# Optimization experiments

Measured on AMD Instinct MI355X. Metric: run time of the kernel, lower is better.

The kernel has to match this reference:

```python
import jax, jax.numpy as jnp
import numpy as np

EPS = 1e-5

def ln(x, g, b):
    m = x.mean(-1, keepdims=True)
    v = ((x - m) ** 2).mean(-1, keepdims=True)
    return (x - m) / jnp.sqrt(v + EPS) * g + b

def mha(x, in_w, in_b, out_w, out_b, nh):
    # Faithful nn.MultiheadAttention with batch_first=False: x is (L, B, D),
    # attention runs over axis 0 (sequence), axis 1 is batch.
    L, Bb, D = x.shape
    hd = D // nh
    qkv = x @ in_w.T + in_b                      # (L, B, 3D)
    q, k, v = jnp.split(qkv, 3, axis=-1)
    q = q.reshape(L, Bb, nh, hd) * (hd ** -0.5)
    k = k.reshape(L, Bb, nh, hd)
    v = v.reshape(L, Bb, nh, hd)
    a = jax.nn.softmax(jnp.einsum('lbhe,sbhe->bhls', q, k), axis=-1)
    o = jnp.einsum('bhls,sbhe->lbhe', a, v).reshape(L, Bb, D)
    return o @ out_w.T + out_b

def psb_forward(features, prev_slots,
                lnq_g, lnq_b, lnkv_g, lnkv_b,
                wq, wk, wv, wo,
                lnt_g, lnt_b, t_in_w, t_in_b, t_out_w, t_out_b,
                lno_g, lno_b, o_in_w, o_in_b, o_out_w, o_out_b,
                lnp_g, lnp_b, w1, b1, w2, b2):
    B, T, L, D = features.shape
    N = prev_slots.shape[2]
    nh = 1                                        # inverse_nh
    hd = D // nh
    slots = ln(prev_slots, lnq_g, lnq_b).reshape(B * T, N, D)
    xkv = ln(features, lnkv_g, lnkv_b).reshape(B * T, L, D)
    # ---- inverse cross attention (softmax over query/slot dim, renorm over keys) ----
    q = (slots @ wq.T).reshape(B * T, N, nh, hd).transpose(0, 2, 1, 3) * (D ** -0.5)
    k = (xkv @ wk.T).reshape(B * T, L, nh, hd).transpose(0, 2, 1, 3)
    v = (xkv @ wv.T).reshape(B * T, L, nh, hd).transpose(0, 2, 1, 3)
    attn = jnp.einsum('bhnd,bhsd->bhns', q, k)    # (BT, nh, N, L)
    attn = jax.nn.softmax(attn, axis=-2)          # over slots (queries)
    attn = attn / attn.sum(-1, keepdims=True)     # renormalize over keys
    s = jnp.einsum('bhns,bhsd->bnhd', attn, v).reshape(B * T, N, D) @ wo.T
    # ---- time attention: input (B*T, N, D); seq axis 0 = B*T, batch = N ----
    s = ln(s, lnt_g, lnt_b)
    s = mha(s, t_in_w, t_in_b, t_out_w, t_out_b, 4)
    # rearrange '(b t) n d -> (b n) t d'
    s = s.reshape(B, T, N, D).transpose(0, 2, 1, 3).reshape(B * N, T, D)
    # ---- object attention: seq axis 0 = B*N, batch = T ----
    s = ln(s, lno_g, lno_b)
    s = mha(s, o_in_w, o_in_b, o_out_w, o_out_b, 4)
    # faithful to torch .view(B, T, N, D) on a contiguous (B*N, T, D) tensor:
    # raw row-major reinterpretation (same as torch)
    s = s.reshape(B, T, N, D)
    # ---- FFN projection + residual with prev_slots ----
    s = ln(s, lnp_g, lnp_b)
    s = jax.nn.relu(s @ w1.T + b1) @ w2.T + b2
    return s + prev_slots

def setup_inputs() -> dict:
    key = jax.random.key(0)
    ks = jax.random.split(key, 16)
    B, T, L, D, N, F = 8, 16, 1024, 192, 8, 512
    w = lambda k, shape: jax.random.normal(k, shape, jnp.float32) * 0.02
    return {
        'features': jax.random.normal(ks[0], (B, T, L, D), jnp.float32),
        'prev_slots': jax.random.normal(ks[1], (B, T, N, D), jnp.float32),
        'lnq_g': jnp.ones((D,), jnp.float32), 'lnq_b': jnp.zeros((D,), jnp.float32),
        'lnkv_g': jnp.ones((D,), jnp.float32), 'lnkv_b': jnp.zeros((D,), jnp.float32),
        'wq': w(ks[2], (D, D)), 'wk': w(ks[3], (D, D)),
        'wv': w(ks[4], (D, D)), 'wo': w(ks[5], (D, D)),
        'lnt_g': jnp.ones((D,), jnp.float32), 'lnt_b': jnp.zeros((D,), jnp.float32),
        't_in_w': w(ks[6], (3 * D, D)), 't_in_b': jnp.zeros((3 * D,), jnp.float32),
        't_out_w': w(ks[7], (D, D)), 't_out_b': jnp.zeros((D,), jnp.float32),
        'lno_g': jnp.ones((D,), jnp.float32), 'lno_b': jnp.zeros((D,), jnp.float32),
        'o_in_w': w(ks[8], (3 * D, D)), 'o_in_b': jnp.zeros((3 * D,), jnp.float32),
        'o_out_w': w(ks[9], (D, D)), 'o_out_b': jnp.zeros((D,), jnp.float32),
        'lnp_g': jnp.ones((D,), jnp.float32), 'lnp_b': jnp.zeros((D,), jnp.float32),
        'w1': w(ks[10], (F, D)), 'b1': jnp.zeros((F,), jnp.float32),
        'w2': w(ks[11], (D, F)), 'b2': jnp.zeros((D,), jnp.float32),
    }

def reference(features, prev_slots,
              lnq_g, lnq_b, lnkv_g, lnkv_b,
              wq, wk, wv, wo,
              lnt_g, lnt_b, t_in_w, t_in_b, t_out_w, t_out_b,
              lno_g, lno_b, o_in_w, o_in_b, o_out_w, o_out_b,
              lnp_g, lnp_b, w1, b1, w2, b2):
    return psb_forward(features, prev_slots,
                       lnq_g, lnq_b, lnkv_g, lnkv_b,
                       wq, wk, wv, wo,
                       lnt_g, lnt_b, t_in_w, t_in_b, t_out_w, t_out_b,
                       lno_g, lno_b, o_in_w, o_in_b, o_out_w, o_out_b,
                       lnp_g, lnp_b, w1, b1, w2, b2)
```

## Files before the change

kernel.cpp:

```cpp
#include <hip/hip_runtime.h>
#include <hip/hip_bf16.h>
#include <stdint.h>

typedef __hip_bfloat16 bf16;

__device__ __forceinline__ float b2f(bf16 x){ return __bfloat162float(x); }
__device__ __forceinline__ bf16  f2b(float x){ return __float2bfloat16(x); }
__device__ __forceinline__ int dflag(const void* rawg){
  return *(const uint32_t*)rawg == 0x3F803F80u;
}

struct Ptrs26 { const void* p[26]; };
__global__ __launch_bounds__(256) void k_convert(Ptrs26 ps, float* __restrict__ dst){
  constexpr int kN[26] = {192,192,192,192, 36864,36864,36864,36864, 192,192,
                          110592,576, 36864,192, 192,192, 110592,576, 36864,192,
                          192,192, 98304,512, 98304,192};
  constexpr int kR[26] = {0,0,0,0, 0,0,0,0, 0,0,
                          576,0, 192,0, 0,0, 576,0, 192,0,
                          0,0, 512,0, 192,0};
  const int b = blockIdx.x;
  int tz = 0, boff = 0, off = 0;
  for (int i = 0; i < 26; ++i){
    const int nb = (kN[i] + 255) >> 8;
    if (b < boff + nb){ tz = i; break; }
    boff += nb; off += kN[i];
  }
  const int cnt = kN[tz];
  const int tid = (b - boff)*256 + threadIdx.x;
  if (tid >= cnt) return;
  const int flag = dflag(ps.p[0]);
  float v = flag ? b2f(((const bf16*)ps.p[tz])[tid]) : ((const float*)ps.p[tz])[tid];
  const int R = kR[tz];
  if (R == 0){
    dst[off + tid] = v;
  } else {
    const int K = cnt / R;
    int o = tid / K, e = tid - o*K;
    dst[off + e*R + o] = v;
  }
}

__global__ __launch_bounds__(192) void k_m1m2(
    const float* __restrict__ wq, const float* __restrict__ wk,
    const float* __restrict__ wo, const float* __restrict__ wv,
    float* __restrict__ M1, float* __restrict__ M2t)
{
  const int t = threadIdx.x, row = blockIdx.x, mat = blockIdx.y;
  float acc = 0.f;
  if (mat == 0){
    for (int d = 0; d < 192; ++d) acc += wq[d*192 + row] * wk[d*192 + t];
    M1[row*192 + t] = acc * 0.07216878364870323f;
  } else {
    for (int d = 0; d < 192; ++d) acc += wo[row*192 + d] * wv[d*192 + t];
    M2t[t*192 + row] = acc;
  }
}

__global__ __launch_bounds__(192) void k_qprime(
    const void* __restrict__ prev, const void* __restrict__ rawg,
    const float* __restrict__ g, const float* __restrict__ be,
    const float* __restrict__ M1, float* __restrict__ Qp)
{
  __shared__ float sRaw[8][196];
  __shared__ float sS[8][196];
  __shared__ float sMS[8][2];
  const int t = threadIdx.x, bt = blockIdx.x;
  const int flag = dflag(rawg);
  #pragma unroll
  for (int r = 0; r < 8; ++r){
    size_t idx = ((size_t)bt*8 + r)*192 + t;
    sRaw[r][t] = flag ? b2f(((const bf16*)prev)[idx]) : ((const float*)prev)[idx];
  }
  __syncthreads();
  if (t < 8){
    float s = 0.f, q = 0.f;
    for (int e = 0; e < 192; ++e){ float x = sRaw[t][e]; s += x; q += x*x; }
    float m = s*(1.f/192.f);
    float rstd = rsqrtf(q*(1.f/192.f) - m*m + 1e-5f);
    sMS[t][0] = m; sMS[t][1] = rstd;
  }
  __syncthreads();
  const float gg = g[t], bb = be[t];
  #pragma unroll
  for (int r = 0; r < 8; ++r)
    sS[r][t] = (sRaw[r][t] - sMS[r][0])*sMS[r][1]*gg + bb;
  __syncthreads();
  float acc[8] = {};
  for (int f = 0; f < 192; ++f){
    float mv = M1[f*192 + t];
    #pragma unroll
    for (int n = 0; n < 8; ++n) acc[n] += sS[n][f]*mv;
  }
  #pragma unroll
  for (int n = 0; n < 8; ++n) Qp[(size_t)bt*1536 + n*192 + t] = acc[n];
}

__global__ __launch_bounds__(256) void k_front(
    const void* __restrict__ feat, const void* __restrict__ rawg,
    const float* __restrict__ g, const float* __restrict__ be,
    const float* __restrict__ Qp, float* __restrict__ pP, float* __restrict__ pR)
{
  __shared__ float sX[16][196];
  __shared__ float sQ[8][196];
  __shared__ float sA[16][9];
  __shared__ float sRS[4][8];
  const int t = threadIdx.x, lane = t & 63, w = t >> 6;
  const int split = blockIdx.x, bt = blockIdx.y;
  const int flag = dflag(rawg);
  const float gg0 = g[lane], gg1 = g[lane+64], gg2 = g[lane+128];
  const float bb0 = be[lane], bb1 = be[lane+64], bb2 = be[lane+128];
  for (int i = t; i < 1536; i += 256){
    int n = i / 192, e = i - n*192;
    sQ[n][e] = Qp[(size_t)bt*1536 + i];
  }
  const int lkey = t >> 4;
  const int lslot = (t >> 1) & 7;
  const int lhalf = t & 1;
  const int pc = t >> 3, pn = t & 7;
  float accP[8] = {0,0,0,0,0,0,0,0};
  float rsAcc = 0.f;
  const size_t rowbase = (size_t)bt*1024 + (size_t)split*64;
  __syncthreads();
  for (int tile = 0; tile < 4; ++tile){
    #pragma unroll
    for (int i = 0; i < 4; ++i){
      int r = w*4 + i;
      size_t ro = (rowbase + tile*16 + r)*192;
      float x0, x1, x2;
      if (flag){
        const bf16* xp = (const bf16*)feat + ro;
        x0 = b2f(xp[lane]); x1 = b2f(xp[lane+64]); x2 = b2f(xp[lane+128]);
      } else {
        const float* xp = (const float*)feat + ro;
        x0 = xp[lane]; x1 = xp[lane+64]; x2 = xp[lane+128];
      }
      float s = x0+x1+x2, q = x0*x0+x1*x1+x2*x2;
      #pragma unroll
      for (int o = 32; o > 0; o >>= 1){ s += __shfl_xor(s,o); q += __shfl_xor(q,o); }
      float m = s*(1.f/192.f);
      float rstd = rsqrtf(q*(1.f/192.f) - m*m + 1e-5f);
      sX[r][lane]     = (x0-m)*rstd*gg0 + bb0;
      sX[r][lane+64]  = (x1-m)*rstd*gg1 + bb1;
      sX[r][lane+128] = (x2-m)*rstd*gg2 + bb2;
    }
    __syncthreads();
    {
      const float* xr = sX[lkey];
      const float* qr = sQ[lslot];
      const int e0 = lhalf*96;
      float acc = 0.f;
      for (int e = e0; e < e0+96; e += 4){
        float4 xv = *(const float4*)(xr + e);
        float4 qv = *(const float4*)(qr + e);
        acc += xv.x*qv.x + xv.y*qv.y + xv.z*qv.z + xv.w*qv.w;
      }
      acc += __shfl_xor(acc, 1);
      float mx = acc;
      mx = fmaxf(mx, __shfl_xor(mx, 2));
      mx = fmaxf(mx, __shfl_xor(mx, 4));
      mx = fmaxf(mx, __shfl_xor(mx, 8));
      float ev = __expf(acc - mx);
      float sum = ev;
      sum += __shfl_xor(sum, 2); sum += __shfl_xor(sum, 4); sum += __shfl_xor(sum, 8);
      float a = ev / sum;
      if (lhalf == 0){ sA[lkey][lslot] = a; rsAcc += a; }
    }
    __syncthreads();
    if (t < 192){
      #pragma unroll 4
      for (int k2 = 0; k2 < 16; ++k2){
        float av = sA[k2][pn];
        const float* xp2 = &sX[k2][pc*8];
        float4 u0 = *(const float4*)(xp2);
        float4 u1 = *(const float4*)(xp2 + 4);
        accP[0] += av*u0.x; accP[1] += av*u0.y; accP[2] += av*u0.z; accP[3] += av*u0.w;
        accP[4] += av*u1.x; accP[5] += av*u1.y; accP[6] += av*u1.z; accP[7] += av*u1.w;
      }
    }
    __syncthreads();
  }
  if (t < 192){
    float* pp = pP + (((size_t)bt*16 + split)*8 + pn)*192 + pc*8;
    *(float4*)pp       = make_float4(accP[0],accP[1],accP[2],accP[3]);
    *(float4*)(pp + 4) = make_float4(accP[4],accP[5],accP[6],accP[7]);
  }
  rsAcc += __shfl_xor(rsAcc, 16);
  rsAcc += __shfl_xor(rsAcc, 32);
  if (lane < 16 && (lane & 1) == 0) sRS[w][lane >> 1] = rsAcc;
  __syncthreads();
  if (t < 8) pR[((size_t)bt*16 + split)*8 + t] = sRS[0][t]+sRS[1][t]+sRS[2][t]+sRS[3][t];
}

__global__ __launch_bounds__(256) void k_finln(
    const float* __restrict__ pP, const float* __restrict__ pR, const float* __restrict__ M2t,
    const float* __restrict__ g, const float* __restrict__ be,
    const float* __restrict__ Wt, const float* __restrict__ bias, float* __restrict__ out)
{
  __shared__ float sP[2][196];
  __shared__ float sx[2][196];
  __shared__ float sInv[2];
  __shared__ float sredS[2][4], sredQ[2][4];
  const int t = threadIdx.x, lane = t & 63, w = t >> 6;
  const int r0 = blockIdx.x*2;
  const int bt = r0 >> 3;
  for (int j = t; j < 384; j += 256){
    int rr = (j >= 192) ? 1 : 0;
    int e = j - rr*192;
    int n = (r0 + rr) & 7;
    const float* src = pP + (((size_t)bt*16)*8 + n)*192 + e;
    float v = 0.f;
    #pragma unroll
    for (int s = 0; s < 16; ++s) v += src[(size_t)s*1536];
    sP[rr][e] = v;
  }
  if (t < 2){
    int n = (r0 + t) & 7;
    float r = 0.f;
    #pragma unroll
    for (int s = 0; s < 16; ++s) r += pR[((size_t)bt*16 + s)*8 + n];
    sInv[t] = 1.f/r;
  }
  __syncthreads();
  float a0 = 0.f, a1 = 0.f;
  if (t < 192){
    for (int e = 0; e < 192; ++e){
      float wv = M2t[e*192 + t];
      a0 += sP[0][e]*wv; a1 += sP[1][e]*wv;
    }
    a0 *= sInv[0]; a1 *= sInv[1];
    float s0 = a0, q0 = a0*a0, s1 = a1, q1 = a1*a1;
    #pragma unroll
    for (int o = 32; o > 0; o >>= 1){
      s0 += __shfl_xor(s0,o); q0 += __shfl_xor(q0,o);
      s1 += __shfl_xor(s1,o); q1 += __shfl_xor(q1,o);
    }
    if (lane == 0){ sredS[0][w]=s0; sredQ[0][w]=q0; sredS[1][w]=s1; sredQ[1][w]=q1; }
  }
  __syncthreads();
  if (t < 192){
    float s0 = sredS[0][0]+sredS[0][1]+sredS[0][2];
    float q0 = sredQ[0][0]+sredQ[0][1]+sredQ[0][2];
    float s1 = sredS[1][0]+sredS[1][1]+sredS[1][2];
    float q1 = sredQ[1][0]+sredQ[1][1]+sredQ[1][2];
    float m0 = s0*(1.f/192.f), m1 = s1*(1.f/192.f);
    float r0s = rsqrtf(q0*(1.f/192.f) - m0*m0 + 1e-5f);
    float r1s = rsqrtf(q1*(1.f/192.f) - m1*m1 + 1e-5f);
    float gg = g[t], bb = be[t];
    sx[0][t] = (a0 - m0)*r0s*gg + bb;
    sx[1][t] = (a1 - m1)*r1s*gg + bb;
  }
  __syncthreads();
  if (t < 192){
    #pragma unroll
    for (int k = 0; k < 3; ++k){
      int o = t + k*192;
      float c0 = bias[o], c1 = bias[o];
      for (int e = 0; e < 192; ++e){
        float wv = Wt[e*576 + o];
        c0 += sx[0][e]*wv; c1 += sx[1][e]*wv;
      }
      out[(size_t)r0*576 + o] = c0;
      out[(size_t)(r0+1)*576 + o] = c1;
    }
  }
}

__global__ __launch_bounds__(256) void k_attn8(
    const float* __restrict__ qkv, float* __restrict__ ao, int S, int B)
{
  __shared__ float sK[128][52];
  __shared__ float sV[128][52];
  __shared__ float sQ[8][52];
  __shared__ float sS[8][132];
  const int t = threadIdx.x;
  const int qt = blockIdx.x, h = blockIdx.y, b = blockIdx.z;
  const float sc = 0.1443375673f;
  for (int i = t; i < S*12; i += 256){
    int ks = i / 12, c = i - ks*12;
    const float* base = qkv + ((size_t)ks*B + b)*576 + h*48 + c*4;
    *(float4*)&sK[ks][c*4] = *(const float4*)(base + 192);
    *(float4*)&sV[ks][c*4] = *(const float4*)(base + 384);
  }
  if (t < 96){
    int qr = t / 12, c = t - qr*12;
    int lq = qt*8 + qr;
    float4 qv = *(const float4*)(qkv + ((size_t)lq*B + b)*576 + h*48 + c*4);
    qv.x *= sc; qv.y *= sc; qv.z *= sc; qv.w *= sc;
    *(float4*)&sQ[qr][c*4] = qv;
  }
  __syncthreads();
  const int qr = t >> 5, kk = t & 31;
  for (int ks = kk; ks < S; ks += 32){
    float acc = 0.f;
    #pragma unroll
    for (int j = 0; j < 12; ++j){
      float4 qv = *(const float4*)&sQ[qr][j*4];
      float4 kv = *(const float4*)&sK[ks][j*4];
      acc += qv.x*kv.x + qv.y*kv.y + qv.z*kv.z + qv.w*kv.w;
    }
    sS[qr][ks] = acc;
  }
  float mx = -1e30f;
  for (int ks = kk; ks < S; ks += 32) mx = fmaxf(mx, sS[qr][ks]);
  #pragma unroll
  for (int m = 1; m < 32; m <<= 1) mx = fmaxf(mx, __shfl_xor(mx, m));
  float sum = 0.f;
  for (int ks = kk; ks < S; ks += 32){
    float e = __expf(sS[qr][ks] - mx);
    sS[qr][ks] = e;
    sum += e;
  }
  #pragma unroll
  for (int m = 1; m < 32; m <<= 1) sum += __shfl_xor(sum, m);
  const float inv = 1.f / sum;
  __syncthreads();
  const int d0 = (kk & 15)*3;
  float a0 = 0.f, a1 = 0.f, a2 = 0.f;
  for (int ks = (kk >> 4); ks < S; ks += 2){
    float p = sS[qr][ks];
    a0 += p*sV[ks][d0]; a1 += p*sV[ks][d0+1]; a2 += p*sV[ks][d0+2];
  }
  a0 += __shfl_xor(a0, 16); a1 += __shfl_xor(a1, 16); a2 += __shfl_xor(a2, 16);
  if (kk < 16){
    const int lq = qt*8 + qr;
    float* op = ao + ((size_t)lq*B + b)*192 + h*48 + d0;
    op[0] = a0*inv; op[1] = a1*inv; op[2] = a2*inv;
  }
}

__global__ __launch_bounds__(256) void k_projln(
    const float* __restrict__ aoT, const float* __restrict__ W1t, const float* __restrict__ b1v,
    const float* __restrict__ g, const float* __restrict__ be,
    const float* __restrict__ Wt, const float* __restrict__ bias, float* __restrict__ out)
{
  __shared__ float sin[2][196];
  __shared__ float sx[2][196];
  __shared__ float sredS[2][4], sredQ[2][4];
  const int t = threadIdx.x, lane = t & 63, w = t >> 6;
  const int r0 = blockIdx.x*2;
  if (t < 192){
    #pragma unroll
    for (int rr = 0; rr < 2; ++rr){
      int r = r0 + rr;
      int ls = r >> 4, tb = r & 15;
      int inrow = ((ls>>3)*16 + tb)*8 + (ls&7);
      sin[rr][t] = aoT[(size_t)inrow*192 + t];
    }
  }
  __syncthreads();
  float a0 = 0.f, a1 = 0.f;
  if (t < 192){
    a0 = b1v[t]; a1 = b1v[t];
    for (int e = 0; e < 192; ++e){
      float wv = W1t[e*192 + t];
      a0 += sin[0][e]*wv; a1 += sin[1][e]*wv;
    }
    float s0 = a0, q0 = a0*a0, s1 = a1, q1 = a1*a1;
    #pragma unroll
    for (int o = 32; o > 0; o >>= 1){
      s0 += __shfl_xor(s0,o); q0 += __shfl_xor(q0,o);
      s1 += __shfl_xor(s1,o); q1 += __shfl_xor(q1,o);
    }
    if (lane == 0){ sredS[0][w]=s0; sredQ[0][w]=q0; sredS[1][w]=s1; sredQ[1][w]=q1; }
  }
  __syncthreads();
  if (t < 192){
    float s0 = sredS[0][0]+sredS[0][1]+sredS[0][2];
    float q0 = sredQ[0][0]+sredQ[0][1]+sredQ[0][2];
    float s1 = sredS[1][0]+sredS[1][1]+sredS[1][2];
    float q1 = sredQ[1][0]+sredQ[1][1]+sredQ[1][2];
    float m0 = s0*(1.f/192.f), m1 = s1*(1.f/192.f);
    float r0s = rsqrtf(q0*(1.f/192.f) - m0*m0 + 1e-5f);
    float r1s = rsqrtf(q1*(1.f/192.f) - m1*m1 + 1e-5f);
    float gg = g[t], bb = be[t];
    sx[0][t] = (a0 - m0)*r0s*gg + bb;
    sx[1][t] = (a1 - m1)*r1s*gg + bb;
  }
  __syncthreads();
  if (t < 192){
    #pragma unroll
    for (int k = 0; k < 3; ++k){
      int o = t + k*192;
      float c0 = bias[o], c1 = bias[o];
      for (int e = 0; e < 192; ++e){
        float wv = Wt[e*576 + o];
        c0 += sx[0][e]*wv; c1 += sx[1][e]*wv;
      }
      out[(size_t)r0*576 + o] = c0;
      out[(size_t)(r0+1)*576 + o] = c1;
    }
  }
}

__global__ __launch_bounds__(256) void k_ffn2(
    const float* __restrict__ aoO, const float* __restrict__ Wpt, const float* __restrict__ bp,
    const float* __restrict__ g, const float* __restrict__ be,
    const float* __restrict__ w1t, const float* __restrict__ b1,
    const float* __restrict__ w2t, const float* __restrict__ b2,
    const void* __restrict__ prev, const void* __restrict__ rawg, void* __restrict__ out)
{
  __shared__ float sin[2][196];
  __shared__ float sx[2][196];
  __shared__ float sh[2][512];
  __shared__ float sredS[2][4], sredQ[2][4];
  const int t = threadIdx.x, lane = t & 63, w = t >> 6;
  const int r0 = blockIdx.x*2;
  const int flag = dflag(rawg);
  if (t < 192){
    sin[0][t] = aoO[(size_t)r0*192 + t];
    sin[1][t] = aoO[(size_t)(r0+1)*192 + t];
  }
  __syncthreads();
  float a0 = 0.f, a1 = 0.f;
  if (t < 192){
    a0 = bp[t]; a1 = bp[t];
    for (int e = 0; e < 192; ++e){
      float wv = Wpt[e*192 + t];
      a0 += sin[0][e]*wv; a1 += sin[1][e]*wv;
    }
    float s0 = a0, q0 = a0*a0, s1 = a1, q1 = a1*a1;
    #pragma unroll
    for (int o = 32; o > 0; o >>= 1){
      s0 += __shfl_xor(s0,o); q0 += __shfl_xor(q0,o);
      s1 += __shfl_xor(s1,o); q1 += __shfl_xor(q1,o);
    }
    if (lane == 0){ sredS[0][w]=s0; sredQ[0][w]=q0; sredS[1][w]=s1; sredQ[1][w]=q1; }
  }
  __syncthreads();
  if (t < 192){
    float s0 = sredS[0][0]+sredS[0][1]+sredS[0][2];
    float q0 = sredQ[0][0]+sredQ[0][1]+sredQ[0][2];
    float s1 = sredS[1][0]+sredS[1][1]+sredS[1][2];
    float q1 = sredQ[1][0]+sredQ[1][1]+sredQ[1][2];
    float m0 = s0*(1.f/192.f), m1 = s1*(1.f/192.f);
    float r0s = rsqrtf(q0*(1.f/192.f) - m0*m0 + 1e-5f);
    float r1s = rsqrtf(q1*(1.f/192.f) - m1*m1 + 1e-5f);
    float gg = g[t], bb = be[t];
    sx[0][t] = (a0 - m0)*r0s*gg + bb;
    sx[1][t] = (a1 - m1)*r1s*gg + bb;
  }
  __syncthreads();
  float h0[2], h1[2];
  {
    float ba = b1[t], bb2v = b1[t+256];
    #pragma unroll
    for (int r = 0; r < 2; ++r){ h0[r]=ba; h1[r]=bb2v; }
  }
  for (int e = 0; e < 192; ++e){
    const float* wr = w1t + e*512;
    float wa = wr[t], wb = wr[t+256];
    #pragma unroll
    for (int r = 0; r < 2; ++r){
      float xv = sx[r][e];
      h0[r] += xv*wa; h1[r] += xv*wb;
    }
  }
  #pragma unroll
  for (int r = 0; r < 2; ++r){
    sh[r][t]     = fmaxf(h0[r], 0.f);
    sh[r][t+256] = fmaxf(h1[r], 0.f);
  }
  __syncthreads();
  if (t < 192){
    float acc[2];
    float bb3 = b2[t];
    acc[0] = bb3; acc[1] = bb3;
    for (int e = 0; e < 512; ++e){
      float wv = w2t[e*192 + t];
      acc[0] += sh[0][e]*wv; acc[1] += sh[1][e]*wv;
    }
    #pragma unroll
    for (int r = 0; r < 2; ++r){
      size_t oi = (size_t)(r0+r)*192 + t;
      float res = flag ? b2f(((const bf16*)prev)[oi]) : ((const float*)prev)[oi];
      float y = acc[r] + res;
      if (flag) ((bf16*)out)[oi] = f2b(y);
      else      ((float*)out)[oi] = y;
    }
  }
}

extern "C" void kernel_launch(void* const* d_in, const int* in_sizes, int n_in,
                              void* d_out, int out_size, void* d_ws, size_t ws_size,
                              hipStream_t stream)
{
  const void* feat = d_in[0];
  const void* prev = d_in[1];
  const void* rawg = d_in[2];
  static const int kWN[26] = {192,192,192,192, 36864,36864,36864,36864, 192,192,
                              110592,576, 36864,192, 192,192, 110592,576, 36864,192,
                              192,192, 98304,512, 98304,192};
  Ptrs26 ps;
  for (int i = 0; i < 26; ++i) ps.p[i] = d_in[2 + i];

  float* wconv = (float*)d_ws;
  size_t woff[26]; size_t acc_ = 0;
  for (int i = 0; i < 26; ++i){ woff[i] = acc_; acc_ += kWN[i]; }
  float* M1   = wconv + 643136;
  float* M2t  = M1 + 36864;
  float* Qp   = M2t + 36864;
  float* pP   = Qp + 196608;
  float* pR   = pP + 3145728;
  float* qkvT = pR + 16384;
  float* aoT  = qkvT + 589824;
  float* qkvO = aoT + 196608;
  float* aoO  = qkvO + 589824;
  const size_t needed = (size_t)((char*)(aoO + 196608) - (char*)d_ws);
  if (ws_size < needed) return;

  const float* c_lnq_g  = wconv + woff[0];
  const float* c_lnq_b  = wconv + woff[1];
  const float* c_lnkv_g = wconv + woff[2];
  const float* c_lnkv_b = wconv + woff[3];
  const float* c_wq     = wconv + woff[4];
  const float* c_wk     = wconv + woff[5];
  const float* c_wv     = wconv + woff[6];
  const float* c_wo     = wconv + woff[7];
  const float* c_lnt_g  = wconv + woff[8];
  const float* c_lnt_b  = wconv + woff[9];
  const float* c_tin_w  = wconv + woff[10];
  const float* c_tin_b  = wconv + woff[11];
  const float* c_tout_w = wconv + woff[12];
  const float* c_tout_b = wconv + woff[13];
  const float* c_lno_g  = wconv + woff[14];
  const float* c_lno_b  = wconv + woff[15];
  const float* c_oin_w  = wconv + woff[16];
  const float* c_oin_b  = wconv + woff[17];
  const float* c_oout_w = wconv + woff[18];
  const float* c_oout_b = wconv + woff[19];
  const float* c_lnp_g  = wconv + woff[20];
  const float* c_lnp_b  = wconv + woff[21];
  const float* c_w1     = wconv + woff[22];
  const float* c_b1     = wconv + woff[23];
  const float* c_w2     = wconv + woff[24];
  const float* c_b2     = wconv + woff[25];

  k_convert<<<2517, 256, 0, stream>>>(ps, wconv);
  k_m1m2<<<dim3(192, 2), 192, 0, stream>>>(c_wq, c_wk, c_wo, c_wv, M1, M2t);
  k_qprime<<<128, 192, 0, stream>>>(prev, rawg, c_lnq_g, c_lnq_b, M1, Qp);
  k_front<<<dim3(16, 128), 256, 0, stream>>>(feat, rawg, c_lnkv_g, c_lnkv_b, Qp, pP, pR);
  k_finln<<<512, 256, 0, stream>>>(pP, pR, M2t, c_lnt_g, c_lnt_b, c_tin_w, c_tin_b, qkvT);
  k_attn8<<<dim3(16,4,8), 256, 0, stream>>>(qkvT, aoT, 128, 8);
  k_projln<<<512, 256, 0, stream>>>(aoT, c_tout_w, c_tout_b, c_lno_g, c_lno_b,
                                    c_oin_w, c_oin_b, qkvO);
  k_attn8<<<dim3(8,4,16), 256, 0, stream>>>(qkvO, aoO, 64, 16);
  k_ffn2<<<512, 256, 0, stream>>>(aoO, c_oout_w, c_oout_b, c_lnp_g, c_lnp_b,
                                  c_w1, c_b1, c_w2, c_b2, prev, rawg, d_out);
}
```

Before: 378.0 us.

## Fold KV layernorm affine into query and output weights, restructure front kernel

Moves the LayerNorm gamma/beta of the key/value features out of the per-row loop. Gamma is folded into the projected query (Qg) and into the pooled values in the finishing kernel, and beta becomes a per-slot score constant (cS) and an output bias (cM2). The front kernel now has 16-lane groups each load a whole row with vector loads, prefetch the next tile, and compute all 8 slot scores per row in registers, cutting shuffles and LDS traffic. The workspace reuses the qkvO and aoO buffers for the new constants, which depends on those buffers being untouched until later stages.

After: 364.9 us. 3.5% less time.

```diff
diff --git a/kernel.cpp b/kernel.cpp
--- a/kernel.cpp
+++ b/kernel.cpp
@@ -6,6 +6,8 @@
 
 __device__ __forceinline__ float b2f(bf16 x){ return __bfloat162float(x); }
 __device__ __forceinline__ bf16  f2b(float x){ return __float2bfloat16(x); }
+__device__ __forceinline__ float bfl(unsigned u){ return __uint_as_float(u << 16); }
+__device__ __forceinline__ float bfh(unsigned u){ return __uint_as_float(u & 0xffff0000u); }
 __device__ __forceinline__ int dflag(const void* rawg){
   return *(const uint32_t*)rawg == 0x3F803F80u;
 }
@@ -43,8 +45,10 @@
 __global__ __launch_bounds__(192) void k_m1m2(
     const float* __restrict__ wq, const float* __restrict__ wk,
     const float* __restrict__ wo, const float* __restrict__ wv,
-    float* __restrict__ M1, float* __restrict__ M2t)
-{
+    const float* __restrict__ bkv,
+    float* __restrict__ M1, float* __restrict__ M2t, float* __restrict__ cM2)
+{
+  __shared__ float sred[3];
   const int t = threadIdx.x, row = blockIdx.x, mat = blockIdx.y;
   float acc = 0.f;
   if (mat == 0){
@@ -53,17 +57,25 @@
   } else {
     for (int d = 0; d < 192; ++d) acc += wo[row*192 + d] * wv[d*192 + t];
     M2t[t*192 + row] = acc;
+    float c = acc * bkv[t];
+    #pragma unroll
+    for (int o = 32; o > 0; o >>= 1) c += __shfl_xor(c, o);
+    if ((t & 63) == 0) sred[t >> 6] = c;
+    __syncthreads();
+    if (t == 0) cM2[row] = sred[0] + sred[1] + sred[2];
   }
 }
 
 __global__ __launch_bounds__(192) void k_qprime(
     const void* __restrict__ prev, const void* __restrict__ rawg,
     const float* __restrict__ g, const float* __restrict__ be,
-    const float* __restrict__ M1, float* __restrict__ Qp)
+    const float* __restrict__ gkv, const float* __restrict__ bkv,
+    const float* __restrict__ M1, float* __restrict__ Qg, float* __restrict__ cS)
 {
   __shared__ float sRaw[8][196];
   __shared__ float sS[8][196];
   __shared__ float sMS[8][2];
+  __shared__ float sCred[3][8];
   const int t = threadIdx.x, bt = blockIdx.x;
   const int flag = dflag(rawg);
   #pragma unroll
@@ -91,81 +103,132 @@
     #pragma unroll
     for (int n = 0; n < 8; ++n) acc[n] += sS[n][f]*mv;
   }
-  #pragma unroll
-  for (int n = 0; n < 8; ++n) Qp[(size_t)bt*1536 + n*192 + t] = acc[n];
+  const float gk = gkv[t], bk = bkv[t];
+  float c[8];
+  #pragma unroll
+  for (int n = 0; n < 8; ++n) c[n] = acc[n]*bk;
+  #pragma unroll
+  for (int o = 32; o > 0; o >>= 1){
+    #pragma unroll
+    for (int n = 0; n < 8; ++n) c[n] += __shfl_xor(c[n], o);
+  }
+  if ((t & 63) == 0){
+    #pragma unroll
+    for (int n = 0; n < 8; ++n) sCred[t >> 6][n] = c[n];
+  }
+  #pragma unroll
+  for (int n = 0; n < 8; ++n) Qg[(size_t)bt*1536 + n*192 + t] = acc[n]*gk;
+  __syncthreads();
+  if (t < 8) cS[(size_t)bt*8 + t] = sCred[0][t] + sCred[1][t] + sCred[2][t];
 }
 
 __global__ __launch_bounds__(256) void k_front(
     const void* __restrict__ feat, const void* __restrict__ rawg,
-    const float* __restrict__ g, const float* __restrict__ be,
-    const float* __restrict__ Qp, float* __restrict__ pP, float* __restrict__ pR)
+    const float* __restrict__ Qg, const float* __restrict__ cSg,
+    float* __restrict__ pP, float* __restrict__ pR)
 {
   __shared__ float sX[16][196];
   __shared__ float sQ[8][196];
-  __shared__ float sA[16][9];
+  __shared__ float sA[16][12];
   __shared__ float sRS[4][8];
+  __shared__ float sCS[8];
   const int t = threadIdx.x, lane = t & 63, w = t >> 6;
   const int split = blockIdx.x, bt = blockIdx.y;
   const int flag = dflag(rawg);
-  const float gg0 = g[lane], gg1 = g[lane+64], gg2 = g[lane+128];
-  const float bb0 = be[lane], bb1 = be[lane+64], bb2 = be[lane+128];
+  const int grp = lane >> 4;
+  const int gl  = lane & 15;
+  const int lrow = w*4 + grp;
+  const int le0  = gl*12;
+  const int pc = t >> 3, pn = t & 7;
+  const size_t rowbase = (size_t)bt*1024 + (size_t)split*64;
+
+  float4 pf0, pf1, pf2;
+  uint2  pb0, pb1, pb2;
+
+  auto issue = [&](int tile){
+    size_t ro = (rowbase + (size_t)(tile*16 + lrow))*192 + le0;
+    if (flag){
+      const uint2* p2 = (const uint2*)((const bf16*)feat + ro);
+      pb0 = p2[0]; pb1 = p2[1]; pb2 = p2[2];
+    } else {
+      const float4* p4 = (const float4*)((const float*)feat + ro);
+      pf0 = p4[0]; pf1 = p4[1]; pf2 = p4[2];
+    }
+  };
+  issue(0);
+
   for (int i = t; i < 1536; i += 256){
     int n = i / 192, e = i - n*192;
-    sQ[n][e] = Qp[(size_t)bt*1536 + i];
-  }
-  const int lkey = t >> 4;
-  const int lslot = (t >> 1) & 7;
-  const int lhalf = t & 1;
-  const int pc = t >> 3, pn = t & 7;
+    sQ[n][e] = Qg[(size_t)bt*1536 + i];
+  }
+  if (t < 8) sCS[t] = cSg[(size_t)bt*8 + t];
+
   float accP[8] = {0,0,0,0,0,0,0,0};
-  float rsAcc = 0.f;
-  const size_t rowbase = (size_t)bt*1024 + (size_t)split*64;
-  __syncthreads();
+  float rs[8]   = {0,0,0,0,0,0,0,0};
+  __syncthreads();
+
   for (int tile = 0; tile < 4; ++tile){
-    #pragma unroll
-    for (int i = 0; i < 4; ++i){
-      int r = w*4 + i;
-      size_t ro = (rowbase + tile*16 + r)*192;
-      float x0, x1, x2;
-      if (flag){
-        const bf16* xp = (const bf16*)feat + ro;
-        x0 = b2f(xp[lane]); x1 = b2f(xp[lane+64]); x2 = b2f(xp[lane+128]);
-      } else {
-        const float* xp = (const float*)feat + ro;
-        x0 = xp[lane]; x1 = xp[lane+64]; x2 = xp[lane+128];
-      }
-      float s = x0+x1+x2, q = x0*x0+x1*x1+x2*x2;
+    float x[12];
+    if (flag){
+      x[0]=bfl(pb0.x); x[1]=bfh(pb0.x); x[2]=bfl(pb0.y); x[3]=bfh(pb0.y);
+      x[4]=bfl(pb1.x); x[5]=bfh(pb1.x); x[6]=bfl(pb1.y); x[7]=bfh(pb1.y);
+      x[8]=bfl(pb2.x); x[9]=bfh(pb2.x); x[10]=bfl(pb2.y); x[11]=bfh(pb2.y);
+    } else {
+      x[0]=pf0.x; x[1]=pf0.y; x[2]=pf0.z; x[3]=pf0.w;
+      x[4]=pf1.x; x[5]=pf1.y; x[6]=pf1.z; x[7]=pf1.w;
+      x[8]=pf2.x; x[9]=pf2.y; x[10]=pf2.z; x[11]=pf2.w;
+    }
+    float s = 0.f, q = 0.f;
+    #pragma unroll
+    for (int j = 0; j < 12; ++j){ s += x[j]; q += x[j]*x[j]; }
+    #pragma unroll
+    for (int o = 1; o < 16; o <<= 1){ s += __shfl_xor(s, o); q += __shfl_xor(q, o); }
+    float m = s*(1.f/192.f);
+    float rstd = rsqrtf(q*(1.f/192.f) - m*m + 1e-5f);
+    *(float4*)&sX[lrow][le0]   = make_float4((x[0]-m)*rstd,(x[1]-m)*rstd,(x[2]-m)*rstd,(x[3]-m)*rstd);
+    *(float4*)&sX[lrow][le0+4] = make_float4((x[4]-m)*rstd,(x[5]-m)*rstd,(x[6]-m)*rstd,(x[7]-m)*rstd);
+    *(float4*)&sX[lrow][le0+8] = make_float4((x[8]-m)*rstd,(x[9]-m)*rstd,(x[10]-m)*rstd,(x[11]-m)*rstd);
+    if (tile < 3) issue(tile + 1);
+    __syncthreads();
+
+    float4 xa = *(const float4*)&sX[lrow][le0];
+    float4 xb = *(const float4*)&sX[lrow][le0+4];
+    float4 xc = *(const float4*)&sX[lrow][le0+8];
+    float p[8];
+    #pragma unroll
+    for (int n = 0; n < 8; ++n){
+      const float* qr = &sQ[n][le0];
+      float4 qa = *(const float4*)qr;
+      float4 qb = *(const float4*)(qr+4);
+      float4 qc = *(const float4*)(qr+8);
+      p[n] = xa.x*qa.x + xa.y*qa.y + xa.z*qa.z + xa.w*qa.w
+           + xb.x*qb.x + xb.y*qb.y + xb.z*qb.z + xb.w*qb.w
+           + xc.x*qc.x + xc.y*qc.y + xc.z*qc.z + xc.w*qc.w;
+    }
+    #pragma unroll
+    for (int o = 1; o < 16; o <<= 1){
       #pragma unroll
-      for (int o = 32; o > 0; o >>= 1){ s += __shfl_xor(s,o); q += __shfl_xor(q,o); }
-      float m = s*(1.f/192.f);
-      float rstd = rsqrtf(q*(1.f/192.f) - m*m + 1e-5f);
-      sX[r][lane]     = (x0-m)*rstd*gg0 + bb0;
-      sX[r][lane+64]  = (x1-m)*rstd*gg1 + bb1;
-      sX[r][lane+128] = (x2-m)*rstd*gg2 + bb2;
+      for (int n = 0; n < 8; ++n) p[n] += __shfl_xor(p[n], o);
+    }
+    #pragma unroll
+    for (int n = 0; n < 8; ++n) p[n] += sCS[n];
+    float mx = p[0];
+    #pragma unroll
+    for (int n = 1; n < 8; ++n) mx = fmaxf(mx, p[n]);
+    float sum = 0.f;
+    #pragma unroll
+    for (int n = 0; n < 8; ++n){ p[n] = __expf(p[n]-mx); sum += p[n]; }
+    float inv = 1.f/sum;
+    #pragma unroll
+    for (int n = 0; n < 8; ++n) p[n] *= inv;
+    if (gl == 0){
+      *(float4*)&sA[lrow][0] = make_float4(p[0],p[1],p[2],p[3]);
+      *(float4*)&sA[lrow][4] = make_float4(p[4],p[5],p[6],p[7]);
+      #pragma unroll
+      for (int n = 0; n < 8; ++n) rs[n] += p[n];
     }
     __syncthreads();
-    {
-      const float* xr = sX[lkey];
-      const float* qr = sQ[lslot];
-      const int e0 = lhalf*96;
-      float acc = 0.f;
-      for (int e = e0; e < e0+96; e += 4){
-        float4 xv = *(const float4*)(xr + e);
-        float4 qv = *(const float4*)(qr + e);
-        acc += xv.x*qv.x + xv.y*qv.y + xv.z*qv.z + xv.w*qv.w;
-      }
-      acc += __shfl_xor(acc, 1);
-      float mx = acc;
-      mx = fmaxf(mx, __shfl_xor(mx, 2));
-      mx = fmaxf(mx, __shfl_xor(mx, 4));
-      mx = fmaxf(mx, __shfl_xor(mx, 8));
-      float ev = __expf(acc - mx);
-      float sum = ev;
-      sum += __shfl_xor(sum, 2); sum += __shfl_xor(sum, 4); sum += __shfl_xor(sum, 8);
-      float a = ev / sum;
-      if (lhalf == 0){ sA[lkey][lslot] = a; rsAcc += a; }
-    }
-    __syncthreads();
+
     if (t < 192){
       #pragma unroll 4
       for (int k2 = 0; k2 < 16; ++k2){
@@ -179,20 +242,28 @@
     }
     __syncthreads();
   }
+
   if (t < 192){
     float* pp = pP + (((size_t)bt*16 + split)*8 + pn)*192 + pc*8;
     *(float4*)pp       = make_float4(accP[0],accP[1],accP[2],accP[3]);
     *(float4*)(pp + 4) = make_float4(accP[4],accP[5],accP[6],accP[7]);
   }
-  rsAcc += __shfl_xor(rsAcc, 16);
-  rsAcc += __shfl_xor(rsAcc, 32);
-  if (lane < 16 && (lane & 1) == 0) sRS[w][lane >> 1] = rsAcc;
+  #pragma unroll
+  for (int n = 0; n < 8; ++n){
+    rs[n] += __shfl_xor(rs[n], 16);
+    rs[n] += __shfl_xor(rs[n], 32);
+  }
+  if (lane == 0){
+    *(float4*)&sRS[w][0] = make_float4(rs[0],rs[1],rs[2],rs[3]);
+    *(float4*)&sRS[w][4] = make_float4(rs[4],rs[5],rs[6],rs[7]);
+  }
   __syncthreads();
   if (t < 8) pR[((size_t)bt*16 + split)*8 + t] = sRS[0][t]+sRS[1][t]+sRS[2][t]+sRS[3][t];
 }
 
 __global__ __launch_bounds__(256) void k_finln(
     const float* __restrict__ pP, const float* __restrict__ pR, const float* __restrict__ M2t,
+    const float* __restrict__ gkv, const float* __restrict__ cM2,
     const float* __restrict__ g, const float* __restrict__ be,
     const float* __restrict__ Wt, const float* __restrict__ bias, float* __restrict__ out)
 {
@@ -211,7 +282,7 @@
     float v = 0.f;
     #pragma unroll
     for (int s = 0; s < 16; ++s) v += src[(size_t)s*1536];
-    sP[rr][e] = v;
+    sP[rr][e] = gkv[e] * v;
   }
   if (t < 2){
     int n = (r0 + t) & 7;
@@ -227,7 +298,8 @@
       float wv = M2t[e*192 + t];
       a0 += sP[0][e]*wv; a1 += sP[1][e]*wv;
     }
-    a0 *= sInv[0]; a1 *= sInv[1];
+    const float cm = cM2[t];
+    a0 = a0*sInv[0] + cm; a1 = a1*sInv[1] + cm;
     float s0 = a0, q0 = a0*a0, s1 = a1, q1 = a1*a1;
     #pragma unroll
     for (int o = 32; o > 0; o >>= 1){
@@ -507,6 +579,8 @@
   float* aoO  = qkvO + 589824;
   const size_t needed = (size_t)((char*)(aoO + 196608) - (char*)d_ws);
   if (ws_size < needed) return;
+  float* cM2 = qkvO;
+  float* cS  = aoO;
 
   const float* c_lnq_g  = wconv + woff[0];
   const float* c_lnq_b  = wconv + woff[1];
@@ -536,10 +610,12 @@
   const float* c_b2     = wconv + woff[25];
 
   k_convert<<<2517, 256, 0, stream>>>(ps, wconv);
-  k_m1m2<<<dim3(192, 2), 192, 0, stream>>>(c_wq, c_wk, c_wo, c_wv, M1, M2t);
-  k_qprime<<<128, 192, 0, stream>>>(prev, rawg, c_lnq_g, c_lnq_b, M1, Qp);
-  k_front<<<dim3(16, 128), 256, 0, stream>>>(feat, rawg, c_lnkv_g, c_lnkv_b, Qp, pP, pR);
-  k_finln<<<512, 256, 0, stream>>>(pP, pR, M2t, c_lnt_g, c_lnt_b, c_tin_w, c_tin_b, qkvT);
+  k_m1m2<<<dim3(192, 2), 192, 0, stream>>>(c_wq, c_wk, c_wo, c_wv, c_lnkv_b, M1, M2t, cM2);
+  k_qprime<<<128, 192, 0, stream>>>(prev, rawg, c_lnq_g, c_lnq_b, c_lnkv_g, c_lnkv_b,
+                                    M1, Qp, cS);
+  k_front<<<dim3(16, 128), 256, 0, stream>>>(feat, rawg, Qp, cS, pP, pR);
+  k_finln<<<512, 256, 0, stream>>>(pP, pR, M2t, c_lnkv_g, cM2, c_lnt_g, c_lnt_b,
+                                   c_tin_w, c_tin_b, qkvT);
   k_attn8<<<dim3(16,4,8), 256, 0, stream>>>(qkvT, aoT, 128, 8);
   k_projln<<<512, 256, 0, stream>>>(aoT, c_tout_w, c_tout_b, c_lno_g, c_lno_b,
                                     c_oin_w, c_oin_b, qkvO);
```
